# Kernel tuning notes

Measured on AMD Instinct MI355X. Metric: run time of the kernel, lower is better.

The kernel has to match this reference:

```python
import jax, jax.numpy as jnp
import numpy as np

N, IC, H, OC, E = 50000, 128, 128, 64, 800000
EPS = 1e-5


def _sage(x, src, dst, wl, wr, b):
    # PyG SAGEConv (mean aggr): out = lin_l(mean_j x_j) + lin_r(x)
    msg = x[src]                                    # [E, d] gather
    s = jax.ops.segment_sum(msg, dst, num_segments=N)
    cnt = jax.ops.segment_sum(jnp.ones((src.shape[0],), x.dtype), dst, num_segments=N)
    mean = s / jnp.clip(cnt, 1.0)[:, None]
    return mean @ wl.T + b + x @ wr.T


def _bn_relu(x, g, be):
    # training-mode BatchNorm1d over node axis (biased var), then ReLU
    m = jnp.mean(x, axis=0)
    v = jnp.mean((x - m) ** 2, axis=0)
    return jax.nn.relu((x - m) * jax.lax.rsqrt(v + EPS) * g + be)


def setup_inputs() -> dict:
    key = jax.random.key(0)
    ks = jax.random.split(key, 16)
    d = {
        "x": jax.random.normal(ks[0], (N, IC), jnp.float32),
        "ei": jax.random.randint(ks[1], (2, E), 0, N, jnp.int32),
        # SAGEConv 1..3: lin_l (with bias) on aggregated, lin_r (no bias) on root
        "w1l": jax.random.normal(ks[2], (H, IC), jnp.float32) / np.sqrt(IC),
        "w1r": jax.random.normal(ks[3], (H, IC), jnp.float32) / np.sqrt(IC),
        "b1c": jnp.zeros((H,), jnp.float32),
        "w2l": jax.random.normal(ks[4], (H, H), jnp.float32) / np.sqrt(H),
        "w2r": jax.random.normal(ks[5], (H, H), jnp.float32) / np.sqrt(H),
        "b2c": jnp.zeros((H,), jnp.float32),
        "w3l": jax.random.normal(ks[6], (H, H), jnp.float32) / np.sqrt(H),
        "w3r": jax.random.normal(ks[7], (H, H), jnp.float32) / np.sqrt(H),
        "b3c": jnp.zeros((H,), jnp.float32),
        # BatchNorm affine params
        "g1": jnp.ones((H,), jnp.float32), "be1": jnp.zeros((H,), jnp.float32),
        "g2": jnp.ones((H,), jnp.float32), "be2": jnp.zeros((H,), jnp.float32),
        "g3": jnp.ones((H,), jnp.float32), "be3": jnp.zeros((H,), jnp.float32),
        # head Linear
        "wh": jax.random.normal(ks[8], (OC, H), jnp.float32) / np.sqrt(H),
        "bh": jnp.zeros((OC,), jnp.float32),
    }
    return d


def reference(x, ei, w1l, w1r, b1c, w2l, w2r, b2c, w3l, w3r, b3c,
              g1, be1, g2, be2, g3, be3, wh, bh):
    src, dst = ei[0], ei[1]
    h = _bn_relu(_sage(x, src, dst, w1l, w1r, b1c), g1, be1)
    # dropout omitted (deterministic reference / eval semantics)
    h = _bn_relu(_sage(h, src, dst, w2l, w2r, b2c), g2, be2)
    h = _bn_relu(_sage(h, src, dst, w3l, w3r, b3c), g3, be3)
    return h @ wh.T + bh
```

## Files before the change

### kernel.cpp

```cpp
#include <hip/hip_runtime.h>

static constexpr int FC = 128;

typedef __attribute__((ext_vector_type(8))) __bf16 bf16x8;
typedef __attribute__((ext_vector_type(4))) float f32x4;

__device__ __forceinline__ unsigned short f2bf(float f) {
  unsigned u = __float_as_uint(f);
  unsigned r = (u + 0x7FFF + ((u >> 16) & 1)) >> 16;
  return (unsigned short)r;
}
__device__ __forceinline__ float bf2f(unsigned short h) {
  return __uint_as_float((unsigned)h << 16);
}

__global__ __launch_bounds__(256) void f2bf_kernel(const float* __restrict__ in,
                                                   unsigned short* __restrict__ out, int n8) {
  int i = blockIdx.x * 256 + threadIdx.x;
  if (i >= n8) return;
  const float* p = in + (size_t)i * 8;
  float4 a = *reinterpret_cast<const float4*>(p);
  float4 b = *reinterpret_cast<const float4*>(p + 4);
  ushort4 o0 = {f2bf(a.x), f2bf(a.y), f2bf(a.z), f2bf(a.w)};
  ushort4 o1 = {f2bf(b.x), f2bf(b.y), f2bf(b.z), f2bf(b.w)};
  unsigned short* q = out + (size_t)i * 8;
  *reinterpret_cast<ushort4*>(q) = o0;
  *reinterpret_cast<ushort4*>(q + 4) = o1;
}

__global__ __launch_bounds__(256) void pack_w_kernel(const float* __restrict__ wl,
                                                     const float* __restrict__ wr,
                                                     unsigned short* __restrict__ out) {
  int i = blockIdx.x * 256 + threadIdx.x;
  int row = i >> 5;
  int k8 = (i & 31) * 8;
  const float* src = (k8 < 128) ? (wl + (size_t)row * 128 + k8)
                                : (wr + (size_t)row * 128 + (k8 - 128));
  float4 a = *reinterpret_cast<const float4*>(src);
  float4 b = *reinterpret_cast<const float4*>(src + 4);
  ushort4 o0 = {f2bf(a.x), f2bf(a.y), f2bf(a.z), f2bf(a.w)};
  ushort4 o1 = {f2bf(b.x), f2bf(b.y), f2bf(b.z), f2bf(b.w)};
  unsigned short* q = out + (size_t)row * 256 + k8;
  *reinterpret_cast<ushort4*>(q) = o0;
  *reinterpret_cast<ushort4*>(q + 4) = o1;
}

__global__ void count_kernel(const int* __restrict__ dst, int* __restrict__ deg,
                             int* __restrict__ rank, int e) {
  int i = blockIdx.x * blockDim.x + threadIdx.x;
  if (i < e) rank[i] = atomicAdd(&deg[dst[i]], 1);
}

__global__ __launch_bounds__(256) void scan1_kernel(const int* __restrict__ deg,
                                                    int* __restrict__ bsum, int n) {
  int i = blockIdx.x * 256 + threadIdx.x;
  int v = (i < n) ? deg[i] : 0;
  __shared__ int ls[256];
  ls[threadIdx.x] = v;
  __syncthreads();
  for (int d = 128; d > 0; d >>= 1) {
    if (threadIdx.x < (unsigned)d) ls[threadIdx.x] += ls[threadIdx.x + d];
    __syncthreads();
  }
  if (threadIdx.x == 0) bsum[blockIdx.x] = ls[0];
}

__global__ __launch_bounds__(256) void scan2_kernel(int* __restrict__ bsum,
                                                    int* __restrict__ off, int n, int nb) {
  __shared__ int ls[256];
  int t = threadIdx.x;
  int v = (t < nb) ? bsum[t] : 0;
  ls[t] = v;
  __syncthreads();
  for (int d = 1; d < 256; d <<= 1) {
    int u = (t >= d) ? ls[t - d] : 0;
    __syncthreads();
    ls[t] += u;
    __syncthreads();
  }
  if (t < nb) bsum[t] = ls[t] - v;
  if (t == 255) off[n] = ls[255];
}

__global__ __launch_bounds__(256) void scan3_kernel(const int* __restrict__ deg,
                                                    const int* __restrict__ bsum,
                                                    int* __restrict__ off, int n) {
  int i = blockIdx.x * 256 + threadIdx.x;
  int t = threadIdx.x;
  int v = (i < n) ? deg[i] : 0;
  __shared__ int ls[256];
  ls[t] = v;
  __syncthreads();
  for (int d = 1; d < 256; d <<= 1) {
    int u = (t >= d) ? ls[t - d] : 0;
    __syncthreads();
    ls[t] += u;
    __syncthreads();
  }
  if (i < n) off[i] = bsum[blockIdx.x] + ls[t] - v;
}

__global__ void fill_kernel(const int* __restrict__ src, const int* __restrict__ dst,
                            const int* __restrict__ rank, const int* __restrict__ off,
                            int* __restrict__ csr, int e) {
  int i = blockIdx.x * blockDim.x + threadIdx.x;
  if (i < e) csr[off[dst[i]] + rank[i]] = src[i];
}

__global__ __launch_bounds__(256) void aggregate_kernel(const unsigned short* __restrict__ x,
                                                        const int* __restrict__ off,
                                                        const int* __restrict__ csr,
                                                        unsigned short* __restrict__ agg, int n) {
  int hw = (int)((blockIdx.x * blockDim.x + threadIdx.x) >> 5);
  int lane = threadIdx.x & 31;
  if (hw >= n) return;
  int s0 = off[hw], s1 = off[hw + 1];
  float a0 = 0.f, a1 = 0.f, a2 = 0.f, a3 = 0.f;
  int j = s0;
  for (; j + 4 <= s1; j += 4) {
    int i0 = csr[j], i1 = csr[j + 1], i2 = csr[j + 2], i3 = csr[j + 3];
    ushort4 v0 = *reinterpret_cast<const ushort4*>(x + (size_t)i0 * FC + lane * 4);
    ushort4 v1 = *reinterpret_cast<const ushort4*>(x + (size_t)i1 * FC + lane * 4);
    ushort4 v2 = *reinterpret_cast<const ushort4*>(x + (size_t)i2 * FC + lane * 4);
    ushort4 v3 = *reinterpret_cast<const ushort4*>(x + (size_t)i3 * FC + lane * 4);
    a0 += (bf2f(v0.x) + bf2f(v1.x)) + (bf2f(v2.x) + bf2f(v3.x));
    a1 += (bf2f(v0.y) + bf2f(v1.y)) + (bf2f(v2.y) + bf2f(v3.y));
    a2 += (bf2f(v0.z) + bf2f(v1.z)) + (bf2f(v2.z) + bf2f(v3.z));
    a3 += (bf2f(v0.w) + bf2f(v1.w)) + (bf2f(v2.w) + bf2f(v3.w));
  }
  for (; j < s1; j++) {
    int i0 = csr[j];
    ushort4 v0 = *reinterpret_cast<const ushort4*>(x + (size_t)i0 * FC + lane * 4);
    a0 += bf2f(v0.x); a1 += bf2f(v0.y); a2 += bf2f(v0.z); a3 += bf2f(v0.w);
  }
  int d = s1 - s0;
  float inv = 1.0f / (float)(d > 0 ? d : 1);
  ushort4 o = {f2bf(a0 * inv), f2bf(a1 * inv), f2bf(a2 * inv), f2bf(a3 * inv)};
  *reinterpret_cast<ushort4*>(agg + (size_t)hw * FC + lane * 4) = o;
}

template <int NCOLS, int KTOT, bool DUAL, bool OUT_BF, bool STATS>
__global__ __launch_bounds__(256) void gemm_kernel(const unsigned short* __restrict__ A1,
                                                   const unsigned short* __restrict__ A2,
                                                   const unsigned short* __restrict__ W,
                                                   const float* __restrict__ bias,
                                                   void* __restrict__ Cout,
                                                   float* __restrict__ stats, int nrows) {
  constexpr int NKT = KTOT / 32;
  constexpr int NCF = NCOLS / 16;
  constexpr int RB = KTOT * 2;
  constexpr int WBYTES = NCOLS * KTOT * 2;
  __shared__ __align__(16) unsigned char Wl[WBYTES];

  int t = threadIdx.x;

  {
    constexpr int CH = WBYTES / 16 / 256;
#pragma unroll
    for (int c = 0; c < CH; c++) {
      int byte = (c * 256 + t) * 16;
      int row = byte / RB;
      int cb = byte % RB;
      float4 v = *reinterpret_cast<const float4*>(reinterpret_cast<const char*>(W) + byte);
      *reinterpret_cast<float4*>(Wl + row * RB + (cb ^ ((row & 7) << 4))) = v;
    }
  }

  int w = t >> 6;
  int l = t & 63;
  int lm = l & 15;
  int hi = l >> 4;
  int lk = hi * 8;
  int row = blockIdx.x * 64 + w * 16 + lm;
  int rclamp = min(row, nrows - 1);

  bf16x8 a[NKT];
#pragma unroll
  for (int kt = 0; kt < NKT; kt++) {
    const unsigned short* Ap;
    int kk;
    if (!DUAL || kt < NKT / 2) { Ap = A1; kk = kt * 32; }
    else                       { Ap = A2; kk = (kt - NKT / 2) * 32; }
    a[kt] = *reinterpret_cast<const bf16x8*>(Ap + (size_t)rclamp * 128 + kk + lk);
  }

  f32x4 acc[NCF];
#pragma unroll
  for (int cf = 0; cf < NCF; cf++) acc[cf] = {0.f, 0.f, 0.f, 0.f};

  __syncthreads();

#pragma unroll
  for (int kt = 0; kt < NKT; kt++) {
#pragma unroll
    for (int cf = 0; cf < NCF; cf++) {
      int r = cf * 16 + lm;
      int cb = kt * 64 + hi * 16;
      bf16x8 b = *reinterpret_cast<const bf16x8*>(Wl + r * RB + (cb ^ ((r & 7) << 4)));
      acc[cf] = __builtin_amdgcn_mfma_f32_16x16x32_bf16(a[kt], b, acc[cf], 0, 0, 0);
    }
  }

  __shared__ float wsum[4][NCOLS];
  __shared__ float wsq[4][NCOLS];

  int orow0 = blockIdx.x * 64 + w * 16 + hi * 4;
#pragma unroll
  for (int cf = 0; cf < NCF; cf++) {
    int col = cf * 16 + lm;
    float bs = bias[col];
    float s = 0.f, s2 = 0.f;
#pragma unroll
    for (int r = 0; r < 4; r++) {
      int orow = orow0 + r;
      bool ok = orow < nrows;
      float v = acc[cf][r] + bs;
      if (ok) {
        if (OUT_BF)
          ((unsigned short*)Cout)[(size_t)orow * NCOLS + col] = f2bf(v);
        else
          ((float*)Cout)[(size_t)orow * NCOLS + col] = v;
      }
      if (STATS) {
        float vv = ok ? v : 0.f;
        s += vv; s2 += vv * vv;
      }
    }
    if (STATS) {
      s  += __shfl_xor(s, 16);  s  += __shfl_xor(s, 32);
      s2 += __shfl_xor(s2, 16); s2 += __shfl_xor(s2, 32);
      if (l < 16) { wsum[w][col] = s; wsq[w][col] = s2; }
    }
  }
  if (STATS) {
    __syncthreads();
    if (t < NCOLS) {
      atomicAdd(&stats[t], wsum[0][t] + wsum[1][t] + wsum[2][t] + wsum[3][t]);
    } else if (t < 2 * NCOLS) {
      int c = t - NCOLS;
      atomicAdd(&stats[t], wsq[0][c] + wsq[1][c] + wsq[2][c] + wsq[3][c]);
    }
  }
}

__global__ __launch_bounds__(256) void bn_apply_kernel(unsigned short* __restrict__ h,
                                                       const float* __restrict__ stats,
                                                       const float* __restrict__ g,
                                                       const float* __restrict__ be,
                                                       float invn, int n) {
  __shared__ float sc[128], sh[128];
  int t = threadIdx.x;
  if (t < 128) {
    float mean = stats[t] * invn;
    float var = fmaxf(stats[128 + t] * invn - mean * mean, 0.f);
    float s = g[t] * rsqrtf(var + 1e-5f);
    sc[t] = s;
    sh[t] = be[t] - mean * s;
  }
  __syncthreads();
  int idx = blockIdx.x * 256 + t;
  if (idx >= n * 16) return;
  int c8 = (idx & 15) * 8;
  unsigned short* p = h + (size_t)idx * 8;
  ushort4 v0 = *reinterpret_cast<const ushort4*>(p);
  ushort4 v1 = *reinterpret_cast<const ushort4*>(p + 4);
  float o[8];
  o[0] = bf2f(v0.x); o[1] = bf2f(v0.y); o[2] = bf2f(v0.z); o[3] = bf2f(v0.w);
  o[4] = bf2f(v1.x); o[5] = bf2f(v1.y); o[6] = bf2f(v1.z); o[7] = bf2f(v1.w);
#pragma unroll
  for (int i = 0; i < 8; i++)
    o[i] = fmaxf(fmaf(o[i], sc[c8 + i], sh[c8 + i]), 0.f);
  ushort4 w0 = {f2bf(o[0]), f2bf(o[1]), f2bf(o[2]), f2bf(o[3])};
  ushort4 w1 = {f2bf(o[4]), f2bf(o[5]), f2bf(o[6]), f2bf(o[7])};
  *reinterpret_cast<ushort4*>(p) = w0;
  *reinterpret_cast<ushort4*>(p + 4) = w1;
}

extern "C" void kernel_launch(void* const* d_in, const int* in_sizes, int n_in,
                              void* d_out, int out_size, void* d_ws, size_t ws_size,
                              hipStream_t stream) {
  const float* x   = (const float*)d_in[0];
  const int*   ei  = (const int*)d_in[1];
  const float* w1l = (const float*)d_in[2];
  const float* w1r = (const float*)d_in[3];
  const float* b1c = (const float*)d_in[4];
  const float* w2l = (const float*)d_in[5];
  const float* w2r = (const float*)d_in[6];
  const float* b2c = (const float*)d_in[7];
  const float* w3l = (const float*)d_in[8];
  const float* w3r = (const float*)d_in[9];
  const float* b3c = (const float*)d_in[10];
  const float* g1  = (const float*)d_in[11];
  const float* be1 = (const float*)d_in[12];
  const float* g2  = (const float*)d_in[13];
  const float* be2 = (const float*)d_in[14];
  const float* g3  = (const float*)d_in[15];
  const float* be3 = (const float*)d_in[16];
  const float* wh  = (const float*)d_in[17];
  const float* bh  = (const float*)d_in[18];

  int n = in_sizes[0] / FC;
  int e = in_sizes[1] / 2;
  const int* srcI = ei;
  const int* dstI = ei + e;

  char* p = (char*)d_ws;
  auto take = [&](size_t bytes) {
    char* q = p;
    p += (bytes + 255) & ~(size_t)255;
    return q;
  };
  int nb = (n + 255) / 256;
  int* deg  = (int*)take((size_t)n * 4);
  int* off  = (int*)take((size_t)(n + 1) * 4);
  int* bsum = (int*)take((size_t)nb * 4);
  int* rank = (int*)take((size_t)e * 4);
  int* csr  = (int*)take((size_t)e * 4);
  unsigned short* x_bf = (unsigned short*)take((size_t)n * FC * 2);
  unsigned short* agg  = (unsigned short*)take((size_t)n * FC * 2);
  unsigned short* h1   = (unsigned short*)take((size_t)n * FC * 2);
  unsigned short* h2   = (unsigned short*)take((size_t)n * FC * 2);
  unsigned short* wc1  = (unsigned short*)take(128 * 256 * 2);
  unsigned short* wc2  = (unsigned short*)take(128 * 256 * 2);
  unsigned short* wc3  = (unsigned short*)take(128 * 256 * 2);
  unsigned short* whb  = (unsigned short*)take(64 * 128 * 2);
  float* stats = (float*)take(3 * 256 * 4);

  float invn = 1.0f / (float)n;

  f2bf_kernel<<<(n * 16 + 255) / 256, 256, 0, stream>>>(x, x_bf, n * 16);
  pack_w_kernel<<<16, 256, 0, stream>>>(w1l, w1r, wc1);
  pack_w_kernel<<<16, 256, 0, stream>>>(w2l, w2r, wc2);
  pack_w_kernel<<<16, 256, 0, stream>>>(w3l, w3r, wc3);
  f2bf_kernel<<<4, 256, 0, stream>>>(wh, whb, 64 * 128 / 8);

  hipMemsetAsync(deg, 0, (size_t)n * 4, stream);
  hipMemsetAsync(stats, 0, 3 * 256 * 4, stream);
  count_kernel<<<(e + 255) / 256, 256, 0, stream>>>(dstI, deg, rank, e);
  scan1_kernel<<<nb, 256, 0, stream>>>(deg, bsum, n);
  scan2_kernel<<<1, 256, 0, stream>>>(bsum, off, n, nb);
  scan3_kernel<<<nb, 256, 0, stream>>>(deg, bsum, off, n);
  fill_kernel<<<(e + 255) / 256, 256, 0, stream>>>(srcI, dstI, rank, off, csr, e);

  auto layer = [&](const unsigned short* in, unsigned short* out, const unsigned short* wc,
                   const float* bc, const float* g, const float* be, float* st) {
    aggregate_kernel<<<(n + 7) / 8, 256, 0, stream>>>(in, off, csr, agg, n);
    gemm_kernel<128, 256, true, true, true><<<(n + 63) / 64, 256, 0, stream>>>(
        agg, in, wc, bc, out, st, n);
    bn_apply_kernel<<<(n * 16 + 255) / 256, 256, 0, stream>>>(out, st, g, be, invn, n);
  };

  layer(x_bf, h1, wc1, b1c, g1, be1, stats);
  layer(h1,   h2, wc2, b2c, g2, be2, stats + 256);
  layer(h2,   h1, wc3, b3c, g3, be3, stats + 512);

  gemm_kernel<64, 128, false, false, false><<<(n + 63) / 64, 256, 0, stream>>>(
      h1, nullptr, whb, bh, d_out, nullptr, n);
}
```

Measured before the change: 289.4 us.

## Fuse BatchNorm+ReLU apply into downstream aggregate and GEMM loads

Removes the three standalone bn_apply passes. Each consumer (neighbor aggregation and the root-input half of the next GEMM, plus the head GEMM) now applies the per-channel scale/shift and ReLU on the fly from the accumulated stats. The two memsets are also replaced by one zero kernel. This saves three full read-modify-write sweeps over the hidden activations. In exchange the BN math is applied per gathered edge in aggregation (about 16x redundant ALU work) and adds a bf16 round-trip in the GEMM A fragments.

After: 276.3 us. -4.5%, faster.

```diff
diff --git a/kernel.cpp b/kernel.cpp
--- a/kernel.cpp
+++ b/kernel.cpp
@@ -12,6 +12,13 @@
 }
 __device__ __forceinline__ float bf2f(unsigned short h) {
   return __uint_as_float((unsigned)h << 16);
+}
+
+__global__ __launch_bounds__(256) void zero_kernel(int* __restrict__ deg,
+                                                   float* __restrict__ stats, int n) {
+  int i = blockIdx.x * 256 + threadIdx.x;
+  if (i < n) deg[i] = 0;
+  if (i < 768) stats[i] = 0.f;
 }
 
 __global__ __launch_bounds__(256) void f2bf_kernel(const float* __restrict__ in,
@@ -107,15 +114,51 @@
   if (i < e) csr[off[dst[i]] + rank[i]] = src[i];
 }
 
+template <bool BNIN>
 __global__ __launch_bounds__(256) void aggregate_kernel(const unsigned short* __restrict__ x,
                                                         const int* __restrict__ off,
                                                         const int* __restrict__ csr,
-                                                        unsigned short* __restrict__ agg, int n) {
+                                                        unsigned short* __restrict__ agg,
+                                                        const float* __restrict__ stats,
+                                                        const float* __restrict__ g,
+                                                        const float* __restrict__ be,
+                                                        float invn, int n) {
   int hw = (int)((blockIdx.x * blockDim.x + threadIdx.x) >> 5);
   int lane = threadIdx.x & 31;
   if (hw >= n) return;
+
+  float sc0 = 1.f, sc1 = 1.f, sc2 = 1.f, sc3 = 1.f;
+  float sh0 = 0.f, sh1 = 0.f, sh2 = 0.f, sh3 = 0.f;
+  if (BNIN) {
+    int c0 = lane * 4;
+    float4 s  = *reinterpret_cast<const float4*>(stats + c0);
+    float4 s2 = *reinterpret_cast<const float4*>(stats + 128 + c0);
+    float4 gv = *reinterpret_cast<const float4*>(g + c0);
+    float4 bv = *reinterpret_cast<const float4*>(be + c0);
+    float m0 = s.x * invn, m1 = s.y * invn, m2 = s.z * invn, m3 = s.w * invn;
+    sc0 = gv.x * rsqrtf(fmaxf(s2.x * invn - m0 * m0, 0.f) + 1e-5f);
+    sc1 = gv.y * rsqrtf(fmaxf(s2.y * invn - m1 * m1, 0.f) + 1e-5f);
+    sc2 = gv.z * rsqrtf(fmaxf(s2.z * invn - m2 * m2, 0.f) + 1e-5f);
+    sc3 = gv.w * rsqrtf(fmaxf(s2.w * invn - m3 * m3, 0.f) + 1e-5f);
+    sh0 = bv.x - m0 * sc0; sh1 = bv.y - m1 * sc1;
+    sh2 = bv.z - m2 * sc2; sh3 = bv.w - m3 * sc3;
+  }
+
   int s0 = off[hw], s1 = off[hw + 1];
   float a0 = 0.f, a1 = 0.f, a2 = 0.f, a3 = 0.f;
+
+#define ACCV(v)                                                          \
+  {                                                                      \
+    float t0 = bf2f((v).x), t1 = bf2f((v).y), t2 = bf2f((v).z), t3 = bf2f((v).w); \
+    if (BNIN) {                                                          \
+      t0 = fmaxf(fmaf(t0, sc0, sh0), 0.f);                               \
+      t1 = fmaxf(fmaf(t1, sc1, sh1), 0.f);                               \
+      t2 = fmaxf(fmaf(t2, sc2, sh2), 0.f);                               \
+      t3 = fmaxf(fmaf(t3, sc3, sh3), 0.f);                               \
+    }                                                                    \
+    a0 += t0; a1 += t1; a2 += t2; a3 += t3;                              \
+  }
+
   int j = s0;
   for (; j + 4 <= s1; j += 4) {
     int i0 = csr[j], i1 = csr[j + 1], i2 = csr[j + 2], i3 = csr[j + 3];
@@ -123,34 +166,38 @@
     ushort4 v1 = *reinterpret_cast<const ushort4*>(x + (size_t)i1 * FC + lane * 4);
     ushort4 v2 = *reinterpret_cast<const ushort4*>(x + (size_t)i2 * FC + lane * 4);
     ushort4 v3 = *reinterpret_cast<const ushort4*>(x + (size_t)i3 * FC + lane * 4);
-    a0 += (bf2f(v0.x) + bf2f(v1.x)) + (bf2f(v2.x) + bf2f(v3.x));
-    a1 += (bf2f(v0.y) + bf2f(v1.y)) + (bf2f(v2.y) + bf2f(v3.y));
-    a2 += (bf2f(v0.z) + bf2f(v1.z)) + (bf2f(v2.z) + bf2f(v3.z));
-    a3 += (bf2f(v0.w) + bf2f(v1.w)) + (bf2f(v2.w) + bf2f(v3.w));
+    ACCV(v0) ACCV(v1) ACCV(v2) ACCV(v3)
   }
   for (; j < s1; j++) {
     int i0 = csr[j];
     ushort4 v0 = *reinterpret_cast<const ushort4*>(x + (size_t)i0 * FC + lane * 4);
-    a0 += bf2f(v0.x); a1 += bf2f(v0.y); a2 += bf2f(v0.z); a3 += bf2f(v0.w);
-  }
+    ACCV(v0)
+  }
+#undef ACCV
+
   int d = s1 - s0;
   float inv = 1.0f / (float)(d > 0 ? d : 1);
   ushort4 o = {f2bf(a0 * inv), f2bf(a1 * inv), f2bf(a2 * inv), f2bf(a3 * inv)};
   *reinterpret_cast<ushort4*>(agg + (size_t)hw * FC + lane * 4) = o;
 }
 
-template <int NCOLS, int KTOT, bool DUAL, bool OUT_BF, bool STATS>
+template <int NCOLS, int KTOT, bool DUAL, bool OUT_BF, bool STATS, bool BNIN>
 __global__ __launch_bounds__(256) void gemm_kernel(const unsigned short* __restrict__ A1,
                                                    const unsigned short* __restrict__ A2,
                                                    const unsigned short* __restrict__ W,
                                                    const float* __restrict__ bias,
                                                    void* __restrict__ Cout,
-                                                   float* __restrict__ stats, int nrows) {
+                                                   float* __restrict__ statsOut,
+                                                   const float* __restrict__ statsIn,
+                                                   const float* __restrict__ g,
+                                                   const float* __restrict__ be,
+                                                   float invn, int nrows) {
   constexpr int NKT = KTOT / 32;
   constexpr int NCF = NCOLS / 16;
   constexpr int RB = KTOT * 2;
   constexpr int WBYTES = NCOLS * KTOT * 2;
   __shared__ __align__(16) unsigned char Wl[WBYTES];
+  __shared__ float scv[128], shv[128];
 
   int t = threadIdx.x;
 
@@ -164,6 +211,14 @@
       float4 v = *reinterpret_cast<const float4*>(reinterpret_cast<const char*>(W) + byte);
       *reinterpret_cast<float4*>(Wl + row * RB + (cb ^ ((row & 7) << 4))) = v;
     }
+  }
+
+  if (BNIN && t < 128) {
+    float mean = statsIn[t] * invn;
+    float var = fmaxf(statsIn[128 + t] * invn - mean * mean, 0.f);
+    float s = g[t] * rsqrtf(var + 1e-5f);
+    scv[t] = s;
+    shv[t] = be[t] - mean * s;
   }
 
   int w = t >> 6;
@@ -189,6 +244,21 @@
   for (int cf = 0; cf < NCF; cf++) acc[cf] = {0.f, 0.f, 0.f, 0.f};
 
   __syncthreads();
+
+  if (BNIN) {
+#pragma unroll
+    for (int kt = 0; kt < NKT; kt++) {
+      if (!DUAL || kt >= NKT / 2) {
+        int ch0 = (DUAL ? (kt - NKT / 2) : kt) * 32 + lk;
+#pragma unroll
+        for (int j = 0; j < 8; j++) {
+          float v = (float)a[kt][j];
+          v = fmaxf(fmaf(v, scv[ch0 + j], shv[ch0 + j]), 0.f);
+          a[kt][j] = (__bf16)v;
+        }
+      }
+    }
+  }
 
 #pragma unroll
   for (int kt = 0; kt < NKT; kt++) {
@@ -235,45 +305,12 @@
   if (STATS) {
     __syncthreads();
     if (t < NCOLS) {
-      atomicAdd(&stats[t], wsum[0][t] + wsum[1][t] + wsum[2][t] + wsum[3][t]);
+      atomicAdd(&statsOut[t], wsum[0][t] + wsum[1][t] + wsum[2][t] + wsum[3][t]);
     } else if (t < 2 * NCOLS) {
       int c = t - NCOLS;
-      atomicAdd(&stats[t], wsq[0][c] + wsq[1][c] + wsq[2][c] + wsq[3][c]);
-    }
-  }
-}
-
-__global__ __launch_bounds__(256) void bn_apply_kernel(unsigned short* __restrict__ h,
-                                                       const float* __restrict__ stats,
-                                                       const float* __restrict__ g,
-                                                       const float* __restrict__ be,
-                                                       float invn, int n) {
-  __shared__ float sc[128], sh[128];
-  int t = threadIdx.x;
-  if (t < 128) {
-    float mean = stats[t] * invn;
-    float var = fmaxf(stats[128 + t] * invn - mean * mean, 0.f);
-    float s = g[t] * rsqrtf(var + 1e-5f);
-    sc[t] = s;
-    sh[t] = be[t] - mean * s;
-  }
-  __syncthreads();
-  int idx = blockIdx.x * 256 + t;
-  if (idx >= n * 16) return;
-  int c8 = (idx & 15) * 8;
-  unsigned short* p = h + (size_t)idx * 8;
-  ushort4 v0 = *reinterpret_cast<const ushort4*>(p);
-  ushort4 v1 = *reinterpret_cast<const ushort4*>(p + 4);
-  float o[8];
-  o[0] = bf2f(v0.x); o[1] = bf2f(v0.y); o[2] = bf2f(v0.z); o[3] = bf2f(v0.w);
-  o[4] = bf2f(v1.x); o[5] = bf2f(v1.y); o[6] = bf2f(v1.z); o[7] = bf2f(v1.w);
-#pragma unroll
-  for (int i = 0; i < 8; i++)
-    o[i] = fmaxf(fmaf(o[i], sc[c8 + i], sh[c8 + i]), 0.f);
-  ushort4 w0 = {f2bf(o[0]), f2bf(o[1]), f2bf(o[2]), f2bf(o[3])};
-  ushort4 w1 = {f2bf(o[4]), f2bf(o[5]), f2bf(o[6]), f2bf(o[7])};
-  *reinterpret_cast<ushort4*>(p) = w0;
-  *reinterpret_cast<ushort4*>(p + 4) = w1;
+      atomicAdd(&statsOut[t], wsq[0][c] + wsq[1][c] + wsq[2][c] + wsq[3][c]);
+    }
+  }
 }
 
 extern "C" void kernel_launch(void* const* d_in, const int* in_sizes, int n_in,
@@ -328,32 +365,36 @@
 
   float invn = 1.0f / (float)n;
 
+  zero_kernel<<<nb, 256, 0, stream>>>(deg, stats, n);
+
   f2bf_kernel<<<(n * 16 + 255) / 256, 256, 0, stream>>>(x, x_bf, n * 16);
   pack_w_kernel<<<16, 256, 0, stream>>>(w1l, w1r, wc1);
   pack_w_kernel<<<16, 256, 0, stream>>>(w2l, w2r, wc2);
   pack_w_kernel<<<16, 256, 0, stream>>>(w3l, w3r, wc3);
   f2bf_kernel<<<4, 256, 0, stream>>>(wh, whb, 64 * 128 / 8);
 
-  hipMemsetAsync(deg, 0, (size_t)n * 4, stream);
-  hipMemsetAsync(stats, 0, 3 * 256 * 4, stream);
   count_kernel<<<(e + 255) / 256, 256, 0, stream>>>(dstI, deg, rank, e);
   scan1_kernel<<<nb, 256, 0, stream>>>(deg, bsum, n);
   scan2_kernel<<<1, 256, 0, stream>>>(bsum, off, n, nb);
   scan3_kernel<<<nb, 256, 0, stream>>>(deg, bsum, off, n);
   fill_kernel<<<(e + 255) / 256, 256, 0, stream>>>(srcI, dstI, rank, off, csr, e);
 
-  auto layer = [&](const unsigned short* in, unsigned short* out, const unsigned short* wc,
-                   const float* bc, const float* g, const float* be, float* st) {
-    aggregate_kernel<<<(n + 7) / 8, 256, 0, stream>>>(in, off, csr, agg, n);
-    gemm_kernel<128, 256, true, true, true><<<(n + 63) / 64, 256, 0, stream>>>(
-        agg, in, wc, bc, out, st, n);
-    bn_apply_kernel<<<(n * 16 + 255) / 256, 256, 0, stream>>>(out, st, g, be, invn, n);
-  };
-
-  layer(x_bf, h1, wc1, b1c, g1, be1, stats);
-  layer(h1,   h2, wc2, b2c, g2, be2, stats + 256);
-  layer(h2,   h1, wc3, b3c, g3, be3, stats + 512);
-
-  gemm_kernel<64, 128, false, false, false><<<(n + 63) / 64, 256, 0, stream>>>(
-      h1, nullptr, whb, bh, d_out, nullptr, n);
-}
+  int gb = (n + 63) / 64;
+  int ab = (n + 7) / 8;
+
+  aggregate_kernel<false><<<ab, 256, 0, stream>>>(x_bf, off, csr, agg, nullptr, nullptr,
+                                                  nullptr, invn, n);
+  gemm_kernel<128, 256, true, true, true, false><<<gb, 256, 0, stream>>>(
+      agg, x_bf, wc1, b1c, h1, stats, nullptr, nullptr, nullptr, invn, n);
+
+  aggregate_kernel<true><<<ab, 256, 0, stream>>>(h1, off, csr, agg, stats, g1, be1, invn, n);
+  gemm_kernel<128, 256, true, true, true, true><<<gb, 256, 0, stream>>>(
+      agg, h1, wc2, b2c, h2, stats + 256, stats, g1, be1, invn, n);
+
+  aggregate_kernel<true><<<ab, 256, 0, stream>>>(h2, off, csr, agg, stats + 256, g2, be2, invn, n);
+  gemm_kernel<128, 256, true, true, true, true><<<gb, 256, 0, stream>>>(
+      agg, h2, wc3, b3c, h1, stats + 512, stats + 256, g2, be2, invn, n);
+
+  gemm_kernel<64, 128, false, false, false, true><<<gb, 256, 0, stream>>>(
+      h1, nullptr, whb, bh, d_out, nullptr, stats + 512, g3, be3, invn, n);
+}
```
